# Optimization experiments

Measured on AMD Instinct MI355X. Metric: run time of the kernel, lower is better.

## Reference

```python
import jax, jax.numpy as jnp
import numpy as np

SLOPE = 0.15  # LeakyReLU negative slope used throughout the module

def leaky(v):
    return jnp.where(v >= 0, v, SLOPE * v)

def _linear_params(key, fan_in, fan_out):
    kw, kb = jax.random.split(key)
    bound = 1.0 / np.sqrt(fan_in)
    W = jax.random.uniform(kw, (fan_in, fan_out), minval=-bound, maxval=bound, dtype=jnp.float32)
    b = jax.random.uniform(kb, (fan_out,), minval=-bound, maxval=bound, dtype=jnp.float32)
    return W, b

N_NODES = 50000
N_EDGES = 640000
IN_DIM = 128
EDGE_DIM = 64
HID = 128
LAT = 64

def setup_inputs() -> dict:
    key = jax.random.key(0)
    ks = jax.random.split(key, 12)
    x = jax.random.normal(ks[0], (N_NODES, IN_DIM), dtype=jnp.float32)
    edge_index = jax.random.randint(ks[1], (2, N_EDGES), 0, N_NODES, dtype=jnp.int32)
    edge_attr = jax.random.normal(ks[2], (N_EDGES, EDGE_DIM), dtype=jnp.float32)
    # conv1 params
    e1W1, e1b1 = _linear_params(ks[3], EDGE_DIM, HID)
    e1W2, e1b2 = _linear_params(ks[4], HID, HID)
    n1W, n1b = _linear_params(ks[5], IN_DIM + HID, HID)
    # conv2 params
    e2W1, e2b1 = _linear_params(ks[6], EDGE_DIM, HID)
    e2W2, e2b2 = _linear_params(ks[7], HID, HID)
    n2W, n2b = _linear_params(ks[8], HID + HID, HID)
    muW, mub = _linear_params(ks[9], HID, LAT)
    lvW, lvb = _linear_params(ks[10], HID, LAT)
    return {"x": x, "edge_index": edge_index, "edge_attr": edge_attr,
            "e1W1": e1W1, "e1b1": e1b1, "e1W2": e1W2, "e1b2": e1b2, "n1W": n1W, "n1b": n1b,
            "e2W1": e2W1, "e2b1": e2b1, "e2W2": e2W2, "e2b2": e2b2, "n2W": n2W, "n2b": n2b,
            "muW": muW, "mub": mub, "lvW": lvW, "lvb": lvb}

def edge_encoder(x, edge_index, edge_attr, eW1, eb1, eW2, eb2, nW, nb):
    # edge MLP: Linear -> LeakyReLU(0.15) -> Linear
    emb = leaky(edge_attr @ eW1 + eb1) @ eW2 + eb2           # [E, H]
    dst = edge_index[1]                                       # PyG x_i = x[target]
    z = jnp.concatenate([x[dst], emb], axis=1)                # [E, in+H]
    msg = z @ nW + nb                                         # [E, H]
    return jax.ops.segment_sum(msg, dst, num_segments=x.shape[0])  # aggr='add'

def reference(x, edge_index, edge_attr,
              e1W1, e1b1, e1W2, e1b2, n1W, n1b,
              e2W1, e2b1, e2W2, e2b2, n2W, n2b,
              muW, mub, lvW, lvb):
    # Dropout is identity in eval mode.
    h = leaky(edge_encoder(x, edge_index, edge_attr, e1W1, e1b1, e1W2, e1b2, n1W, n1b))
    h = leaky(edge_encoder(h, edge_index, edge_attr, e2W1, e2b1, e2W2, e2b2, n2W, n2b))
    mu = h @ muW + mub
    logvar = h @ lvW + lvb
    return (mu, logvar)
```

## Files before the change

kernel.cpp:

```cpp
#include <hip/hip_runtime.h>

typedef __bf16 bf16x4 __attribute__((ext_vector_type(4)));
typedef __bf16 bf16x8 __attribute__((ext_vector_type(8)));
typedef float  f32x4  __attribute__((ext_vector_type(4)));

constexpr int N_NODES = 50000;
constexpr int N_EDGES = 640000;
constexpr int NTILES  = 98;

__device__ __forceinline__ float leaky(float v) { return v >= 0.f ? v : 0.15f * v; }

__global__ void prep_kernel(
    const float* __restrict__ e1W1, const float* __restrict__ e1b1,
    const float* __restrict__ e1W2, const float* __restrict__ e1b2,
    const float* __restrict__ n1W,  const float* __restrict__ n1b,
    const float* __restrict__ e2W1, const float* __restrict__ e2b1,
    const float* __restrict__ e2W2, const float* __restrict__ e2b2,
    const float* __restrict__ n2W,  const float* __restrict__ n2b,
    const float* __restrict__ muW,  const float* __restrict__ mub,
    const float* __restrict__ lvW,  const float* __restrict__ lvb,
    __bf16* __restrict__ packE, __bf16* __restrict__ packN1,
    __bf16* __restrict__ packN2, __bf16* __restrict__ packH,
    float* __restrict__ ebias, float* __restrict__ c1, float* __restrict__ c2,
    float* __restrict__ hbias)
{
    int bid = blockIdx.x;
    int lane = threadIdx.x;
    int quad = lane >> 4, low = lane & 15;

    if (bid < 32) {
        int ct = bid >> 1, kt = bid & 1;
        for (int j = 0; j < 8; ++j) {
            int k = kt * 32 + quad * 8 + j;
            int n = ct * 16 + low;
            float v = (n < 128) ? e1W1[k * 128 + n] : e2W1[k * 128 + (n - 128)];
            packE[((ct * 2 + kt) * 64 + lane) * 8 + j] = (__bf16)v;
        }
    } else if (bid < 160) {
        bool is1 = bid < 96;
        int tile = bid - (is1 ? 32 : 96);
        const float* nW  = is1 ? n1W  : n2W;
        const float* eW2 = is1 ? e1W2 : e2W2;
        __bf16* dst = is1 ? packN1 : packN2;
        int ct = tile >> 3, kt = tile & 7;
        for (int j = 0; j < 8; ++j) {
            int k = kt * 32 + quad * 8 + j;
            int n = ct * 16 + low;
            float v;
            if (k < 128) {
                v = nW[k * 128 + n];
            } else {
                int i = k - 128;
                float acc = 0.f;
                for (int k2 = 0; k2 < 128; ++k2)
                    acc += eW2[i * 128 + k2] * nW[(128 + k2) * 128 + n];
                v = acc;
            }
            dst[((ct * 8 + kt) * 64 + lane) * 8 + j] = (__bf16)v;
        }
    } else if (bid < 192) {
        int tile = bid - 160;
        int ct = tile >> 2, kt = tile & 3;
        for (int j = 0; j < 8; ++j) {
            int k = kt * 32 + quad * 8 + j;
            int n = ct * 16 + low;
            float v = (n < 64) ? muW[k * 64 + n] : lvW[k * 64 + (n - 64)];
            packH[((ct * 4 + kt) * 64 + lane) * 8 + j] = (__bf16)v;
        }
    } else if (bid == 192 || bid == 193) {
        const float* nW  = (bid == 192) ? n1W  : n2W;
        const float* nb  = (bid == 192) ? n1b  : n2b;
        const float* eb2 = (bid == 192) ? e1b2 : e2b2;
        float* dst = (bid == 192) ? c1 : c2;
        for (int rep = 0; rep < 2; ++rep) {
            int j = lane + rep * 64;
            float acc = nb[j];
            for (int k = 0; k < 128; ++k)
                acc += eb2[k] * nW[(128 + k) * 128 + j];
            dst[j] = acc;
        }
    } else {
        for (int rep = 0; rep < 4; ++rep) {
            int j = lane + rep * 64;
            ebias[j] = (j < 128) ? e1b1[j] : e2b1[j - 128];
        }
        for (int rep = 0; rep < 2; ++rep) {
            int j = lane + rep * 64;
            hbias[j] = (j < 64) ? mub[j] : lvb[j - 64];
        }
    }
}

__global__ void hist_kernel(const int* __restrict__ dstp, int* __restrict__ deg) {
    int e = blockIdx.x * 256 + threadIdx.x;
    if (e < N_EDGES) atomicAdd(&deg[dstp[e]], 1);
}

__global__ void scan_a(const int* __restrict__ deg, int* __restrict__ offs,
                       int* __restrict__ tileSum) {
    __shared__ int s[512];
    int t = threadIdx.x, i = blockIdx.x * 512 + t;
    int v = (i < N_NODES) ? deg[i] : 0;
    s[t] = v; __syncthreads();
    for (int off = 1; off < 512; off <<= 1) {
        int x = (t >= off) ? s[t - off] : 0;
        __syncthreads();
        s[t] += x;
        __syncthreads();
    }
    if (i < N_NODES) offs[i] = s[t] - v;
    if (t == 511) tileSum[blockIdx.x] = s[511];
}

__global__ void scan_b(const int* __restrict__ tileSum, int* __restrict__ tileOff) {
    __shared__ int s[128];
    int t = threadIdx.x;
    int v = (t < NTILES) ? tileSum[t] : 0;
    s[t] = v; __syncthreads();
    for (int off = 1; off < 128; off <<= 1) {
        int x = (t >= off) ? s[t - off] : 0;
        __syncthreads();
        s[t] += x;
        __syncthreads();
    }
    if (t < NTILES) tileOff[t] = s[t] - v;
}

__global__ void scan_c(int* __restrict__ offs, const int* __restrict__ tileOff,
                       const int* __restrict__ deg, float* __restrict__ degf) {
    int i = blockIdx.x * 256 + threadIdx.x;
    if (i < N_NODES) {
        offs[i] += tileOff[i >> 9];
        degf[i] = (float)deg[i];
    }
}

__global__ void scatter_kernel(const int* __restrict__ dstp, const int* __restrict__ offs,
                               int* __restrict__ cursor, int* __restrict__ sorted) {
    int e = blockIdx.x * 256 + threadIdx.x;
    if (e < N_EDGES) {
        int d = dstp[e];
        int p = offs[d] + atomicAdd(&cursor[d], 1);
        sorted[p] = e;
    }
}

__global__ __launch_bounds__(256, 3) void edge_kernel(
    const float* __restrict__ edge_attr, const int* __restrict__ dstp,
    const int* __restrict__ sorted, const __bf16* __restrict__ packE,
    const float* __restrict__ ebias, float* __restrict__ S)
{
    __shared__ alignas(16) __bf16 As[64 * 72];
    __shared__ alignas(16) __bf16 Lball[4 * 64 * 72];
    __shared__ int eidx_s[64];
    __shared__ alignas(8) unsigned char runof_s[64];
    __shared__ int rundst_s[64];
    __shared__ int nruns_s;

    int tid = threadIdx.x;
    int e0 = blockIdx.x * 64;

    int myd = 0;
    if (tid < 64) {
        int ei = sorted[e0 + tid];
        eidx_s[tid] = ei;
        myd = dstp[ei];
    }
    __syncthreads();

    {
        int r = tid >> 2, c0 = (tid & 3) * 16;
        const float4* src = reinterpret_cast<const float4*>(
            edge_attr + (size_t)eidx_s[r] * 64 + c0);
        float4 f0 = src[0], f1 = src[1], f2 = src[2], f3 = src[3];
        bf16x8 v0, v1;
        v0[0]=(__bf16)f0.x; v0[1]=(__bf16)f0.y; v0[2]=(__bf16)f0.z; v0[3]=(__bf16)f0.w;
        v0[4]=(__bf16)f1.x; v0[5]=(__bf16)f1.y; v0[6]=(__bf16)f1.z; v0[7]=(__bf16)f1.w;
        v1[0]=(__bf16)f2.x; v1[1]=(__bf16)f2.y; v1[2]=(__bf16)f2.z; v1[3]=(__bf16)f2.w;
        v1[4]=(__bf16)f3.x; v1[5]=(__bf16)f3.y; v1[6]=(__bf16)f3.z; v1[7]=(__bf16)f3.w;
        *reinterpret_cast<bf16x8*>(&As[r * 72 + c0])     = v0;
        *reinterpret_cast<bf16x8*>(&As[r * 72 + c0 + 8]) = v1;
    }

    if (tid < 64) {
        rundst_s[tid] = myd;
        int dp = __shfl_up(myd, 1);
        bool flag = (tid > 0) && (myd != dp);
        unsigned long long mask = __ballot(flag);
        int rid = __popcll(mask & ((1ull << tid) - 1ull)) + (flag ? 1 : 0);
        runof_s[tid] = (unsigned char)rid;
        if (flag || tid == 0) rundst_s[rid] = myd;
        if (tid == 0) nruns_s = __popcll(mask) + 1;
    }
    __syncthreads();

    int w = tid >> 6, lane = tid & 63;
    int quad = lane >> 4, low = lane & 15;

    f32x4 C1[4][4] = {};
    #pragma unroll
    for (int kt = 0; kt < 2; ++kt) {
        bf16x8 bf[4];
        #pragma unroll
        for (int ct = 0; ct < 4; ++ct)
            bf[ct] = *reinterpret_cast<const bf16x8*>(
                packE + (((w * 4 + ct) * 2 + kt) * 64 + lane) * 8);
        #pragma unroll
        for (int rt = 0; rt < 4; ++rt) {
            bf16x8 a = *reinterpret_cast<const bf16x8*>(
                &As[(rt * 16 + low) * 72 + kt * 32 + quad * 8]);
            #pragma unroll
            for (int ct = 0; ct < 4; ++ct)
                C1[rt][ct] = __builtin_amdgcn_mfma_f32_16x16x32_bf16(a, bf[ct], C1[rt][ct], 0, 0, 0);
        }
    }

    __bf16* Lb = &Lball[w * 4608];
    float bias_c[4];
    #pragma unroll
    for (int ct = 0; ct < 4; ++ct) bias_c[ct] = ebias[w * 64 + ct * 16 + low];

    #pragma unroll
    for (int rt = 0; rt < 4; ++rt)
        #pragma unroll
        for (int ct = 0; ct < 4; ++ct) {
            bf16x4 v;
            #pragma unroll
            for (int r = 0; r < 4; ++r)
                v[r] = (__bf16)leaky(C1[rt][ct][r] + bias_c[ct]);
            *reinterpret_cast<bf16x4*>(
                &Lb[(ct * 16 + low) * 72 + rt * 16 + quad * 4]) = v;
        }
    __syncthreads();

    int nruns = nruns_s;
    for (int rt2 = 0; rt2 * 16 < nruns; ++rt2) {
        f32x4 C2[4] = {};
        #pragma unroll
        for (int kt = 0; kt < 2; ++kt) {
            uint2 rb = *reinterpret_cast<const uint2*>(&runof_s[kt * 32 + quad * 8]);
            unsigned target = (unsigned)(rt2 * 16 + low);
            bf16x8 a;
            #pragma unroll
            for (int j = 0; j < 8; ++j) {
                unsigned byte = ((j < 4 ? (rb.x >> (8 * j)) : (rb.y >> (8 * (j - 4)))) & 0xFFu);
                a[j] = (byte == target) ? (__bf16)1.0f : (__bf16)0.0f;
            }
            #pragma unroll
            for (int ct = 0; ct < 4; ++ct) {
                bf16x8 b = *reinterpret_cast<const bf16x8*>(
                    &Lb[(ct * 16 + low) * 72 + kt * 32 + quad * 8]);
                C2[ct] = __builtin_amdgcn_mfma_f32_16x16x32_bf16(a, b, C2[ct], 0, 0, 0);
            }
        }
        #pragma unroll
        for (int ct = 0; ct < 4; ++ct) {
            int col = w * 64 + ct * 16 + low;
            #pragma unroll
            for (int r = 0; r < 4; ++r) {
                int run = rt2 * 16 + quad * 4 + r;
                if (run < nruns) {
                    int node = rundst_s[run];
                    if ((unsigned)node < (unsigned)N_NODES)
                        unsafeAtomicAdd(&S[(size_t)node * 256 + col], C2[ct][r]);
                }
            }
        }
    }
}

template<int KT, int KT1, bool SCALE, bool ACT, bool SPLIT>
__global__ __launch_bounds__(256) void node_gemm(
    const float* __restrict__ A1, int lda1,
    const float* __restrict__ A2, int lda2,
    const float* __restrict__ degf,
    const __bf16* __restrict__ Bpack, const float* __restrict__ bias,
    float* __restrict__ out)
{
    int w = threadIdx.x >> 6, lane = threadIdx.x & 63;
    int quad = lane >> 4, low = lane & 15;
    int rb = blockIdx.x * 64 + w * 16;

    int arow = rb + low;
    if (arow >= N_NODES) arow = N_NODES - 1;
    float s = 1.f;
    if (SCALE) s = degf[arow];

    f32x4 C[8] = {};
    #pragma unroll
    for (int kt = 0; kt < KT; ++kt) {
        const float* base;
        if (kt < KT1) base = A1 + (size_t)arow * lda1 + kt * 32 + quad * 8;
        else          base = A2 + (size_t)arow * lda2 + (kt - KT1) * 32 + quad * 8;
        float4 p0 = *reinterpret_cast<const float4*>(base);
        float4 p1 = *reinterpret_cast<const float4*>(base + 4);
        float m = (SCALE && kt < KT1) ? s : 1.f;
        bf16x8 a;
        a[0] = (__bf16)(p0.x * m); a[1] = (__bf16)(p0.y * m);
        a[2] = (__bf16)(p0.z * m); a[3] = (__bf16)(p0.w * m);
        a[4] = (__bf16)(p1.x * m); a[5] = (__bf16)(p1.y * m);
        a[6] = (__bf16)(p1.z * m); a[7] = (__bf16)(p1.w * m);
        #pragma unroll
        for (int ct = 0; ct < 8; ++ct) {
            bf16x8 b = *reinterpret_cast<const bf16x8*>(Bpack + ((ct * KT + kt) * 64 + lane) * 8);
            C[ct] = __builtin_amdgcn_mfma_f32_16x16x32_bf16(a, b, C[ct], 0, 0, 0);
        }
    }

    #pragma unroll
    for (int ct = 0; ct < 8; ++ct) {
        int col = ct * 16 + low;
        #pragma unroll
        for (int r = 0; r < 4; ++r) {
            int row = rb + quad * 4 + r;
            if (row >= N_NODES) continue;
            float bb = bias[col];
            if (SCALE) bb *= degf[row];
            float v = C[ct][r] + bb;
            if (ACT) v = leaky(v);
            if (SPLIT) {
                if (col < 64) out[(size_t)row * 64 + col] = v;
                else          out[(size_t)N_NODES * 64 + (size_t)row * 64 + (col - 64)] = v;
            } else {
                out[(size_t)row * 128 + col] = v;
            }
        }
    }
}

extern "C" void kernel_launch(void* const* d_in, const int* in_sizes, int n_in,
                              void* d_out, int out_size, void* d_ws, size_t ws_size,
                              hipStream_t stream)
{
    const float* x     = (const float*)d_in[0];
    const int*   eidx  = (const int*)  d_in[1];
    const float* eattr = (const float*)d_in[2];
    const float* e1W1 = (const float*)d_in[3];
    const float* e1b1 = (const float*)d_in[4];
    const float* e1W2 = (const float*)d_in[5];
    const float* e1b2 = (const float*)d_in[6];
    const float* n1W  = (const float*)d_in[7];
    const float* n1b  = (const float*)d_in[8];
    const float* e2W1 = (const float*)d_in[9];
    const float* e2b1 = (const float*)d_in[10];
    const float* e2W2 = (const float*)d_in[11];
    const float* e2b2 = (const float*)d_in[12];
    const float* n2W  = (const float*)d_in[13];
    const float* n2b  = (const float*)d_in[14];
    const float* muW  = (const float*)d_in[15];
    const float* mub  = (const float*)d_in[16];
    const float* lvW  = (const float*)d_in[17];
    const float* lvb  = (const float*)d_in[18];

    const int* dstp = eidx + N_EDGES;

    char* ws = (char*)d_ws;
    size_t off = 0;
    auto alloc = [&](size_t bytes) -> void* {
        void* p = ws + off;
        off = (off + bytes + 1023) & ~(size_t)1023;
        return p;
    };
    float* S       = (float*)alloc((size_t)N_NODES * 256 * 4);
    float* h       = (float*)alloc((size_t)N_NODES * 128 * 4);
    float* g       = (float*)alloc((size_t)N_NODES * 128 * 4);
    int*   deg     = (int*)  alloc((size_t)N_NODES * 4);
    int*   cursor  = (int*)  alloc((size_t)N_NODES * 4);
    int*   offs    = (int*)  alloc((size_t)N_NODES * 4);
    float* degf    = (float*)alloc((size_t)N_NODES * 4);
    int*   sorted  = (int*)  alloc((size_t)N_EDGES * 4);
    int*   tileSum = (int*)  alloc(NTILES * 4);
    int*   tileOff = (int*)  alloc(NTILES * 4);
    __bf16* packE  = (__bf16*)alloc(32 * 64 * 8 * 2);
    __bf16* packN1 = (__bf16*)alloc(64 * 64 * 8 * 2);
    __bf16* packN2 = (__bf16*)alloc(64 * 64 * 8 * 2);
    __bf16* packH  = (__bf16*)alloc(32 * 64 * 8 * 2);
    float* ebias   = (float*)alloc(256 * 4);
    float* c1      = (float*)alloc(128 * 4);
    float* c2      = (float*)alloc(128 * 4);
    float* hbias   = (float*)alloc(128 * 4);
    (void)ws_size; (void)in_sizes; (void)n_in; (void)out_size;

    hipMemsetAsync(S,      0, (size_t)N_NODES * 256 * 4, stream);
    hipMemsetAsync(deg,    0, (size_t)N_NODES * 4, stream);
    hipMemsetAsync(cursor, 0, (size_t)N_NODES * 4, stream);

    prep_kernel<<<195, 64, 0, stream>>>(e1W1, e1b1, e1W2, e1b2, n1W, n1b,
                                        e2W1, e2b1, e2W2, e2b2, n2W, n2b,
                                        muW, mub, lvW, lvb,
                                        packE, packN1, packN2, packH,
                                        ebias, c1, c2, hbias);

    hist_kernel<<<N_EDGES / 256, 256, 0, stream>>>(dstp, deg);
    scan_a<<<NTILES, 512, 0, stream>>>(deg, offs, tileSum);
    scan_b<<<1, 128, 0, stream>>>(tileSum, tileOff);
    scan_c<<<(N_NODES + 255) / 256, 256, 0, stream>>>(offs, tileOff, deg, degf);
    scatter_kernel<<<N_EDGES / 256, 256, 0, stream>>>(dstp, offs, cursor, sorted);

    edge_kernel<<<N_EDGES / 64, 256, 0, stream>>>(eattr, dstp, sorted, packE, ebias, S);

    node_gemm<8, 4, true, true, false><<<(N_NODES + 63) / 64, 256, 0, stream>>>(
        x, 128, S, 256, degf, packN1, c1, h);
    node_gemm<8, 4, true, true, false><<<(N_NODES + 63) / 64, 256, 0, stream>>>(
        h, 128, S + 128, 256, degf, packN2, c2, g);
    node_gemm<4, 4, false, false, true><<<(N_NODES + 63) / 64, 256, 0, stream>>>(
        g, 128, g, 128, degf, packH, hbias, (float*)d_out);
}
```

Before: 559.1 us.

## Make edge kernel persistent with software-prefetched edge tiles and sorted dst array

```diff
diff --git a/kernel.cpp b/kernel.cpp
--- a/kernel.cpp
+++ b/kernel.cpp
@@ -7,6 +7,7 @@
 constexpr int N_NODES = 50000;
 constexpr int N_EDGES = 640000;
 constexpr int NTILES  = 98;
+constexpr int NB_EDGE = 2500;
 
 __device__ __forceinline__ float leaky(float v) { return v >= 0.f ? v : 0.15f * v; }
 
@@ -136,136 +137,161 @@
 }
 
 __global__ void scatter_kernel(const int* __restrict__ dstp, const int* __restrict__ offs,
-                               int* __restrict__ cursor, int* __restrict__ sorted) {
+                               int* __restrict__ cursor, int* __restrict__ sorted,
+                               int* __restrict__ sdst) {
     int e = blockIdx.x * 256 + threadIdx.x;
     if (e < N_EDGES) {
         int d = dstp[e];
         int p = offs[d] + atomicAdd(&cursor[d], 1);
         sorted[p] = e;
+        sdst[p] = d;
     }
 }
 
 __global__ __launch_bounds__(256, 3) void edge_kernel(
-    const float* __restrict__ edge_attr, const int* __restrict__ dstp,
-    const int* __restrict__ sorted, const __bf16* __restrict__ packE,
+    const float* __restrict__ edge_attr,
+    const int* __restrict__ sorted, const int* __restrict__ sdst,
+    const __bf16* __restrict__ packE,
     const float* __restrict__ ebias, float* __restrict__ S)
 {
     __shared__ alignas(16) __bf16 As[64 * 72];
     __shared__ alignas(16) __bf16 Lball[4 * 64 * 72];
-    __shared__ int eidx_s[64];
     __shared__ alignas(8) unsigned char runof_s[64];
     __shared__ int rundst_s[64];
     __shared__ int nruns_s;
 
     int tid = threadIdx.x;
-    int e0 = blockIdx.x * 64;
-
-    int myd = 0;
-    if (tid < 64) {
-        int ei = sorted[e0 + tid];
-        eidx_s[tid] = ei;
-        myd = dstp[ei];
-    }
-    __syncthreads();
-
-    {
-        int r = tid >> 2, c0 = (tid & 3) * 16;
-        const float4* src = reinterpret_cast<const float4*>(
-            edge_attr + (size_t)eidx_s[r] * 64 + c0);
-        float4 f0 = src[0], f1 = src[1], f2 = src[2], f3 = src[3];
-        bf16x8 v0, v1;
-        v0[0]=(__bf16)f0.x; v0[1]=(__bf16)f0.y; v0[2]=(__bf16)f0.z; v0[3]=(__bf16)f0.w;
-        v0[4]=(__bf16)f1.x; v0[5]=(__bf16)f1.y; v0[6]=(__bf16)f1.z; v0[7]=(__bf16)f1.w;
-        v1[0]=(__bf16)f2.x; v1[1]=(__bf16)f2.y; v1[2]=(__bf16)f2.z; v1[3]=(__bf16)f2.w;
-        v1[4]=(__bf16)f3.x; v1[5]=(__bf16)f3.y; v1[6]=(__bf16)f3.z; v1[7]=(__bf16)f3.w;
-        *reinterpret_cast<bf16x8*>(&As[r * 72 + c0])     = v0;
-        *reinterpret_cast<bf16x8*>(&As[r * 72 + c0 + 8]) = v1;
-    }
-
-    if (tid < 64) {
-        rundst_s[tid] = myd;
-        int dp = __shfl_up(myd, 1);
-        bool flag = (tid > 0) && (myd != dp);
-        unsigned long long mask = __ballot(flag);
-        int rid = __popcll(mask & ((1ull << tid) - 1ull)) + (flag ? 1 : 0);
-        runof_s[tid] = (unsigned char)rid;
-        if (flag || tid == 0) rundst_s[rid] = myd;
-        if (tid == 0) nruns_s = __popcll(mask) + 1;
-    }
-    __syncthreads();
-
     int w = tid >> 6, lane = tid & 63;
     int quad = lane >> 4, low = lane & 15;
-
-    f32x4 C1[4][4] = {};
+    int r = tid >> 2, c0 = (tid & 3) * 16;
+
+    bf16x8 bfragE[2][4];
     #pragma unroll
-    for (int kt = 0; kt < 2; ++kt) {
-        bf16x8 bf[4];
+    for (int kt = 0; kt < 2; ++kt)
         #pragma unroll
         for (int ct = 0; ct < 4; ++ct)
-            bf[ct] = *reinterpret_cast<const bf16x8*>(
+            bfragE[kt][ct] = *reinterpret_cast<const bf16x8*>(
                 packE + (((w * 4 + ct) * 2 + kt) * 64 + lane) * 8);
-        #pragma unroll
-        for (int rt = 0; rt < 4; ++rt) {
-            bf16x8 a = *reinterpret_cast<const bf16x8*>(
-                &As[(rt * 16 + low) * 72 + kt * 32 + quad * 8]);
-            #pragma unroll
-            for (int ct = 0; ct < 4; ++ct)
-                C1[rt][ct] = __builtin_amdgcn_mfma_f32_16x16x32_bf16(a, bf[ct], C1[rt][ct], 0, 0, 0);
-        }
-    }
-
-    __bf16* Lb = &Lball[w * 4608];
     float bias_c[4];
     #pragma unroll
     for (int ct = 0; ct < 4; ++ct) bias_c[ct] = ebias[w * 64 + ct * 16 + low];
 
-    #pragma unroll
-    for (int rt = 0; rt < 4; ++rt)
+    __bf16* Lb = &Lball[w * 4608];
+
+    constexpr int STRIDE = NB_EDGE * 64;
+    int e0 = blockIdx.x * 64;
+
+    float4 f0, f1, f2, f3;
+    int md_c, ei_n, md_n;
+    {
+        int ei = sorted[e0 + r];
+        md_c = sdst[e0 + lane];
+        const float4* ap = reinterpret_cast<const float4*>(edge_attr + (size_t)ei * 64 + c0);
+        f0 = ap[0]; f1 = ap[1]; f2 = ap[2]; f3 = ap[3];
+    }
+    ei_n = sorted[e0 + STRIDE + r];
+    md_n = sdst[e0 + STRIDE + lane];
+
+    #pragma unroll 1
+    for (int it = 0; it < 4; ++it) {
+        {
+            bf16x8 v0, v1;
+            v0[0]=(__bf16)f0.x; v0[1]=(__bf16)f0.y; v0[2]=(__bf16)f0.z; v0[3]=(__bf16)f0.w;
+            v0[4]=(__bf16)f1.x; v0[5]=(__bf16)f1.y; v0[6]=(__bf16)f1.z; v0[7]=(__bf16)f1.w;
+            v1[0]=(__bf16)f2.x; v1[1]=(__bf16)f2.y; v1[2]=(__bf16)f2.z; v1[3]=(__bf16)f2.w;
+            v1[4]=(__bf16)f3.x; v1[5]=(__bf16)f3.y; v1[6]=(__bf16)f3.z; v1[7]=(__bf16)f3.w;
+            *reinterpret_cast<bf16x8*>(&As[r * 72 + c0])     = v0;
+            *reinterpret_cast<bf16x8*>(&As[r * 72 + c0 + 8]) = v1;
+        }
+
+        if (w == 0) {
+            rundst_s[lane] = md_c;
+            int dp = __shfl_up(md_c, 1);
+            bool flag = (lane > 0) && (md_c != dp);
+            unsigned long long mask = __ballot(flag);
+            int rid = __popcll(mask & ((1ull << lane) - 1ull)) + (flag ? 1 : 0);
+            runof_s[lane] = (unsigned char)rid;
+            if (flag || lane == 0) rundst_s[rid] = md_c;
+            if (lane == 0) nruns_s = __popcll(mask) + 1;
+        }
+        __syncthreads();
+
+        float4 g0{}, g1{}, g2{}, g3{};
+        if (it < 3) {
+            const float4* gp = reinterpret_cast<const float4*>(
+                edge_attr + (size_t)ei_n * 64 + c0);
+            g0 = gp[0]; g1 = gp[1]; g2 = gp[2]; g3 = gp[3];
+        }
+        int ei_nn = 0, md_nn = 0;
+        if (it < 2) {
+            int eo = e0 + (it + 2) * STRIDE;
+            ei_nn = sorted[eo + r];
+            md_nn = sdst[eo + lane];
+        }
+
+        f32x4 C1[4][4] = {};
         #pragma unroll
-        for (int ct = 0; ct < 4; ++ct) {
-            bf16x4 v;
+        for (int kt = 0; kt < 2; ++kt)
             #pragma unroll
-            for (int r = 0; r < 4; ++r)
-                v[r] = (__bf16)leaky(C1[rt][ct][r] + bias_c[ct]);
-            *reinterpret_cast<bf16x4*>(
-                &Lb[(ct * 16 + low) * 72 + rt * 16 + quad * 4]) = v;
-        }
-    __syncthreads();
-
-    int nruns = nruns_s;
-    for (int rt2 = 0; rt2 * 16 < nruns; ++rt2) {
-        f32x4 C2[4] = {};
+            for (int rt = 0; rt < 4; ++rt) {
+                bf16x8 a = *reinterpret_cast<const bf16x8*>(
+                    &As[(rt * 16 + low) * 72 + kt * 32 + quad * 8]);
+                #pragma unroll
+                for (int ct = 0; ct < 4; ++ct)
+                    C1[rt][ct] = __builtin_amdgcn_mfma_f32_16x16x32_bf16(
+                        a, bfragE[kt][ct], C1[rt][ct], 0, 0, 0);
+            }
+
         #pragma unroll
-        for (int kt = 0; kt < 2; ++kt) {
-            uint2 rb = *reinterpret_cast<const uint2*>(&runof_s[kt * 32 + quad * 8]);
-            unsigned target = (unsigned)(rt2 * 16 + low);
-            bf16x8 a;
-            #pragma unroll
-            for (int j = 0; j < 8; ++j) {
-                unsigned byte = ((j < 4 ? (rb.x >> (8 * j)) : (rb.y >> (8 * (j - 4)))) & 0xFFu);
-                a[j] = (byte == target) ? (__bf16)1.0f : (__bf16)0.0f;
-            }
+        for (int rt = 0; rt < 4; ++rt)
             #pragma unroll
             for (int ct = 0; ct < 4; ++ct) {
-                bf16x8 b = *reinterpret_cast<const bf16x8*>(
-                    &Lb[(ct * 16 + low) * 72 + kt * 32 + quad * 8]);
-                C2[ct] = __builtin_amdgcn_mfma_f32_16x16x32_bf16(a, b, C2[ct], 0, 0, 0);
-            }
-        }
-        #pragma unroll
-        for (int ct = 0; ct < 4; ++ct) {
-            int col = w * 64 + ct * 16 + low;
+                bf16x4 v;
+                #pragma unroll
+                for (int rr = 0; rr < 4; ++rr)
+                    v[rr] = (__bf16)leaky(C1[rt][ct][rr] + bias_c[ct]);
+                *reinterpret_cast<bf16x4*>(
+                    &Lb[(ct * 16 + low) * 72 + rt * 16 + quad * 4]) = v;
+            }
+
+        int nruns = nruns_s;
+        for (int rt2 = 0; rt2 * 16 < nruns; ++rt2) {
+            f32x4 C2[4] = {};
             #pragma unroll
-            for (int r = 0; r < 4; ++r) {
-                int run = rt2 * 16 + quad * 4 + r;
-                if (run < nruns) {
-                    int node = rundst_s[run];
-                    if ((unsigned)node < (unsigned)N_NODES)
-                        unsafeAtomicAdd(&S[(size_t)node * 256 + col], C2[ct][r]);
+            for (int kt = 0; kt < 2; ++kt) {
+                uint2 rb = *reinterpret_cast<const uint2*>(&runof_s[kt * 32 + quad * 8]);
+                unsigned target = (unsigned)(rt2 * 16 + low);
+                bf16x8 a;
+                #pragma unroll
+                for (int j = 0; j < 8; ++j) {
+                    unsigned byte = ((j < 4 ? (rb.x >> (8 * j)) : (rb.y >> (8 * (j - 4)))) & 0xFFu);
+                    a[j] = (byte == target) ? (__bf16)1.0f : (__bf16)0.0f;
                 }
-            }
-        }
+                #pragma unroll
+                for (int ct = 0; ct < 4; ++ct) {
+                    bf16x8 b = *reinterpret_cast<const bf16x8*>(
+                        &Lb[(ct * 16 + low) * 72 + kt * 32 + quad * 8]);
+                    C2[ct] = __builtin_amdgcn_mfma_f32_16x16x32_bf16(a, b, C2[ct], 0, 0, 0);
+                }
+            }
+            #pragma unroll
+            for (int ct = 0; ct < 4; ++ct) {
+                int col = w * 64 + ct * 16 + low;
+                #pragma unroll
+                for (int rr = 0; rr < 4; ++rr) {
+                    int run = rt2 * 16 + quad * 4 + rr;
+                    if (run < nruns) {
+                        int node = rundst_s[run];
+                        if ((unsigned)node < (unsigned)N_NODES)
+                            unsafeAtomicAdd(&S[(size_t)node * 256 + col], C2[ct][rr]);
+                    }
+                }
+            }
+        }
+        __syncthreads();
+
+        f0 = g0; f1 = g1; f2 = g2; f3 = g3;
+        md_c = md_n; ei_n = ei_nn; md_n = md_nn;
     }
 }
 
@@ -311,12 +337,12 @@
     for (int ct = 0; ct < 8; ++ct) {
         int col = ct * 16 + low;
         #pragma unroll
-        for (int r = 0; r < 4; ++r) {
-            int row = rb + quad * 4 + r;
+        for (int rr = 0; rr < 4; ++rr) {
+            int row = rb + quad * 4 + rr;
             if (row >= N_NODES) continue;
             float bb = bias[col];
             if (SCALE) bb *= degf[row];
-            float v = C[ct][r] + bb;
+            float v = C[ct][rr] + bb;
             if (ACT) v = leaky(v);
             if (SPLIT) {
                 if (col < 64) out[(size_t)row * 64 + col] = v;
@@ -381,9 +407,10 @@
     float* hbias   = (float*)alloc(128 * 4);
     (void)ws_size; (void)in_sizes; (void)n_in; (void)out_size;
 
-    hipMemsetAsync(S,      0, (size_t)N_NODES * 256 * 4, stream);
-    hipMemsetAsync(deg,    0, (size_t)N_NODES * 4, stream);
-    hipMemsetAsync(cursor, 0, (size_t)N_NODES * 4, stream);
+    int* sdst = (int*)g;
+
+    hipMemsetAsync(S, 0, (size_t)N_NODES * 256 * 4, stream);
+    hipMemsetAsync(deg, 0, 2 * (((size_t)N_NODES * 4 + 1023) & ~(size_t)1023), stream);
 
     prep_kernel<<<195, 64, 0, stream>>>(e1W1, e1b1, e1W2, e1b2, n1W, n1b,
                                         e2W1, e2b1, e2W2, e2b2, n2W, n2b,
@@ -395,9 +422,9 @@
     scan_a<<<NTILES, 512, 0, stream>>>(deg, offs, tileSum);
     scan_b<<<1, 128, 0, stream>>>(tileSum, tileOff);
     scan_c<<<(N_NODES + 255) / 256, 256, 0, stream>>>(offs, tileOff, deg, degf);
-    scatter_kernel<<<N_EDGES / 256, 256, 0, stream>>>(dstp, offs, cursor, sorted);
-
-    edge_kernel<<<N_EDGES / 64, 256, 0, stream>>>(eattr, dstp, sorted, packE, ebias, S);
+    scatter_kernel<<<N_EDGES / 256, 256, 0, stream>>>(dstp, offs, cursor, sorted, sdst);
+
+    edge_kernel<<<NB_EDGE, 256, 0, stream>>>(eattr, sorted, sdst, packE, ebias, S);
 
     node_gemm<8, 4, true, true, false><<<(N_NODES + 63) / 64, 256, 0, stream>>>(
         x, 128, S, 256, degf, packN1, c1, h);
```

Result: faster. 490.4 us (-12.3%).
